# Optimization experiments

Hardware: AMD Instinct MI355X
Metric: run time of the kernel (lower is better)

## Reference

```python
import jax, jax.numpy as jnp
import numpy as np

I = 2048  # input_size
O = 2048  # output_size
K = 16    # number of parallel linears

def setup_inputs() -> dict:
    key = jax.random.key(0)
    ks = jax.random.split(key, 8)
    s_in = 1.0 / np.sqrt(I)
    s_cat = 1.0 / np.sqrt(K * O)
    x = jax.random.normal(ks[0], (4, 2048, I), dtype=jnp.float32)
    W16 = jax.random.uniform(ks[1], (K, O, I), jnp.float32, -s_in, s_in)   # stacked weights of 16 Linears
    b16 = jax.random.uniform(ks[2], (K, O), jnp.float32, -s_in, s_in)
    Wf = jax.random.uniform(ks[3], (O, K * O), jnp.float32, -s_cat, s_cat)  # fusion Linear weight
    bf = jax.random.uniform(ks[4], (O,), jnp.float32, -s_cat, s_cat)
    gamma = jnp.ones((O,), jnp.float32)  # LayerNorm weight
    beta = jnp.zeros((O,), jnp.float32)  # LayerNorm bias
    return {"x": x, "W16": W16, "b16": b16, "Wf": Wf, "bf": bf, "gamma": gamma, "beta": beta}

def reference(x, W16, b16, Wf, bf, gamma, beta):
    B, S, _ = x.shape
    # 16 parallel Linears as one batched GEMM; k index order == torch.cat order
    y = jnp.einsum('bsi,koi->bsko', x, W16) + b16          # [B,S,16,O]
    combined = y.reshape(B, S, K * O)                       # concat along last dim
    fused = jnp.einsum('bsc,oc->bso', combined, Wf) + bf    # fusion linear [B,S,O]
    # LayerNorm (eps=1e-5, torch default)
    mu = jnp.mean(fused, axis=-1, keepdims=True)
    var = jnp.mean(jnp.square(fused - mu), axis=-1, keepdims=True)
    normed = (fused - mu) * jax.lax.rsqrt(var + 1e-5) * gamma + beta
    # exact (erf) GELU matching torch nn.GELU default; dropout(p=0.005) is identity at eval
    return jax.nn.gelu(normed, approximate=False)
```

## Files before the change

kernel.cpp:

```cpp
#include <hip/hip_runtime.h>
#include <hip/hip_bf16.h>
#include <math.h>


typedef __bf16 bf16_t;
typedef __bf16 bf16x8 __attribute__((ext_vector_type(8)));
typedef __bf16 bf16x4 __attribute__((ext_vector_type(4)));
typedef float  f32x4  __attribute__((ext_vector_type(4)));

#define KC 32768
#define OD 2048
#define ID 2048
#define BSROWS 8192

#define GLL16(g, l) __builtin_amdgcn_global_load_lds( \
    (const __attribute__((address_space(1))) void*)(g), \
    (__attribute__((address_space(3))) void*)(l), 16, 0, 0)

__device__ __forceinline__ float wave_sum(float v) {
#pragma unroll
  for (int o = 32; o > 0; o >>= 1) v += __shfl_down(v, o, 64);
  return v;
}

__global__ __launch_bounds__(512, 1) void gemm256(
    const bf16_t* __restrict__ A, const bf16_t* __restrict__ B,
    float* __restrict__ C, int M, int N, int lda, int ldb,
    int Ks, int nbn, int mn)
{
  __shared__ char lds[131072];
  const int tid  = threadIdx.x;
  const int lane = tid & 63;
  const int wave = tid >> 6;

  const int nwg = gridDim.x;
  const int per = nwg >> 3;
  const int swz = (blockIdx.x & 7) * per + (blockIdx.x >> 3);
  const int z   = swz / mn;
  const int rem = swz - z * mn;
  const int bm  = (rem / nbn) * 256;
  const int bn  = (rem % nbn) * 256;
  const int k0  = z * Ks;
  float* Cz = C + (size_t)z * ((size_t)M * (size_t)N);

  const int wr = wave >> 2, wc = wave & 3;
  const int frow  = lane & 15;
  const int bhalf = wc >> 1;

  const int rdsl0 = (((lane >> 4))     ^ (lane & 7)) * 16;
  const int rdsl1 = (((lane >> 4) + 4) ^ (lane & 7)) * 16;

  const int abase = wr * 16384 + frow * 128;
  const int bloc  = ((wc & 1) * 64 + frow) * 128;

  const int srow8 = tid >> 3;
  const int sw8   = (tid & 7) ^ (srow8 & 7);
  const bf16_t* gA0 = A + (size_t)(bm + srow8) * lda + k0 + sw8 * 8;
  const bf16_t* gB0 = B + (size_t)(bn + srow8) * ldb + k0 + sw8 * 8;
  const int ldw = wave * 1024;

  f32x4 acc[8][4] = {};
  bf16x8 aqE[2][2], aqO[2][2], bA[4][2], bB[4][2];
  const int NT = Ks >> 6;

#define STAGE_A_HALF(t, hf) do {                                          \
    _Pragma("unroll") for (int s_ = 0; s_ < 2; ++s_)                      \
      GLL16(gA0 + (size_t)((hf) * 128 + s_ * 64) * lda + (size_t)(t) * 64,\
            lds + (((t) & 1) << 15) + (hf) * 16384 + s_ * 8192 + ldw);    \
  } while (0)

#define STAGE_B_HALF(t, hh) do {                                          \
    _Pragma("unroll") for (int s_ = 0; s_ < 2; ++s_)                      \
      GLL16(gB0 + (size_t)((hh) * 128 + s_ * 64) * ldb + (size_t)(t) * 64,\
            lds + 65536 + ((((t) * 2 + (hh)) & 3) << 14) + s_ * 8192 + ldw); \
  } while (0)

#define READ_AQ(t, q, aq) do {                                            \
    const char* p_ = lds + (((t) & 1) << 15) + abase + (q) * 4096;        \
    aq[0][0] = *reinterpret_cast<const bf16x8*>(p_ + rdsl0);              \
    aq[0][1] = *reinterpret_cast<const bf16x8*>(p_ + rdsl1);              \
    aq[1][0] = *reinterpret_cast<const bf16x8*>(p_ + 2048 + rdsl0);       \
    aq[1][1] = *reinterpret_cast<const bf16x8*>(p_ + 2048 + rdsl1);       \
  } while (0)

#define READ_BH(t, kh, bg) do {                                           \
    const char* p_ = lds + 65536 + ((((t) * 2 + bhalf) & 3) << 14) + bloc;\
    _Pragma("unroll") for (int n_ = 0; n_ < 4; ++n_)                      \
      bg[n_][kh] = *reinterpret_cast<const bf16x8*>(                      \
          p_ + n_ * 2048 + ((kh) ? rdsl1 : rdsl0));                       \
  } while (0)

#define SYNCPH() do {                                                     \
    __builtin_amdgcn_s_barrier();                                         \
    asm volatile("s_waitcnt lgkmcnt(0)" ::: "memory");                    \
    __builtin_amdgcn_sched_barrier(0);                                    \
  } while (0)

#define MFMA_Q(q, aq, bg) do {                                            \
    __builtin_amdgcn_s_setprio(1);                                        \
    _Pragma("unroll") for (int mh_ = 0; mh_ < 2; ++mh_)                   \
      _Pragma("unroll") for (int n_ = 0; n_ < 4; ++n_) {                  \
        acc[2*(q)+mh_][n_] = __builtin_amdgcn_mfma_f32_16x16x32_bf16(     \
            aq[mh_][0], bg[n_][0], acc[2*(q)+mh_][n_], 0, 0, 0);          \
        acc[2*(q)+mh_][n_] = __builtin_amdgcn_mfma_f32_16x16x32_bf16(     \
            aq[mh_][1], bg[n_][1], acc[2*(q)+mh_][n_], 0, 0, 0);          \
      }                                                                   \
    __builtin_amdgcn_s_setprio(0);                                        \
  } while (0)

#define TILE(t, BC, BN) do {                                              \
                                                                  \
    if ((t) + 1 < NT) { STAGE_A_HALF((t) + 1, 0); STAGE_A_HALF((t) + 1, 1); } \
    READ_AQ((t), 0, aqE);                                                 \
    SYNCPH(); MFMA_Q(0, aqE, BC);                                         \
                                                                  \
    READ_AQ((t), 1, aqO);                                                 \
    SYNCPH(); MFMA_Q(1, aqO, BC);                                         \
    if ((t) + 1 < NT) {                  \
      asm volatile("s_waitcnt vmcnt(4)" ::: "memory");                    \
      __builtin_amdgcn_s_barrier();                                       \
    }                                                                     \
                                                                  \
    if ((t) + 2 < NT) { STAGE_B_HALF((t) + 2, 0); STAGE_B_HALF((t) + 2, 1); } \
    READ_AQ((t), 2, aqE);                                                 \
    if ((t) + 1 < NT) READ_BH((t) + 1, 0, BN);                            \
    SYNCPH(); MFMA_Q(2, aqE, BC);                                         \
                                                                  \
    READ_AQ((t), 3, aqO);                                                 \
    if ((t) + 1 < NT) READ_BH((t) + 1, 1, BN);                            \
    SYNCPH(); MFMA_Q(3, aqO, BC);                                         \
    if ((t) + 2 < NT) {                  \
      asm volatile("s_waitcnt vmcnt(4)" ::: "memory");                    \
      __builtin_amdgcn_s_barrier();                                       \
    } else if ((t) + 1 < NT) {                                            \
      asm volatile("s_waitcnt vmcnt(0)" ::: "memory");    \
      __builtin_amdgcn_s_barrier();                                       \
    }                                                                     \
  } while (0)

  STAGE_A_HALF(0, 0); STAGE_A_HALF(0, 1);
  STAGE_B_HALF(0, 0); STAGE_B_HALF(0, 1);
  STAGE_B_HALF(1, 0); STAGE_B_HALF(1, 1);
  asm volatile("s_waitcnt vmcnt(4)" ::: "memory");
  __builtin_amdgcn_s_barrier();
  READ_BH(0, 0, bA);
  READ_BH(0, 1, bA);
  asm volatile("s_waitcnt lgkmcnt(0)" ::: "memory");
  __builtin_amdgcn_sched_barrier(0);
  __builtin_amdgcn_s_barrier();

#pragma unroll 1
  for (int t = 0; t < NT; t += 2) {
    TILE(t,     bA, bB);
    TILE(t + 1, bB, bA);
  }
#undef TILE
#undef MFMA_Q
#undef SYNCPH
#undef READ_BH
#undef READ_AQ
#undef STAGE_B_HALF
#undef STAGE_A_HALF

  const int wrbase = wr * 128, wcbase = wc * 64;
  const int cr = (lane >> 4) * 4, cc = lane & 15;
#pragma unroll
  for (int m = 0; m < 8; ++m)
#pragma unroll
    for (int n = 0; n < 4; ++n) {
      size_t base = (size_t)(bm + wrbase + m * 16 + cr) * N + (bn + wcbase + n * 16 + cc);
#pragma unroll
      for (int j = 0; j < 4; ++j)
        Cz[base + (size_t)j * N] = acc[m][n][j];
    }
}

#define PREP_WF_BLOCKS   32768
#define PREP_TR_BLOCKS   16384
#define PREP_X_BLOCKS    8192
#define PREP_TOTAL       (PREP_WF_BLOCKS + PREP_TR_BLOCKS + PREP_X_BLOCKS)

__global__ __launch_bounds__(256) void prep_all(
    const float* __restrict__ Wf, const float* __restrict__ b16,
    const float* __restrict__ W16, const float* __restrict__ X,
    bf16_t* __restrict__ Wf16, bf16_t* __restrict__ W16T,
    bf16_t* __restrict__ X16, float* __restrict__ beq)
{
  __shared__ bf16_t tile[64][65];
  const int b = blockIdx.x;
  const int t = threadIdx.x;

  if (b < PREP_WF_BLOCKS) {
    const int o  = b >> 4;
    const int cb = (b & 15) * 2048;
    const size_t gbase = (size_t)o * KC + cb + t * 8;
    const float4 v0 = *(const float4*)(Wf + gbase);
    const float4 v1 = *(const float4*)(Wf + gbase + 4);
    const float4 b0 = *(const float4*)(b16 + cb + t * 8);
    const float4 b1 = *(const float4*)(b16 + cb + t * 8 + 4);
    bf16x8 r;
    r[0] = (bf16_t)v0.x; r[1] = (bf16_t)v0.y; r[2] = (bf16_t)v0.z; r[3] = (bf16_t)v0.w;
    r[4] = (bf16_t)v1.x; r[5] = (bf16_t)v1.y; r[6] = (bf16_t)v1.z; r[7] = (bf16_t)v1.w;
    *reinterpret_cast<bf16x8*>(Wf16 + gbase) = r;
    float s = v0.x * b0.x + v0.y * b0.y + v0.z * b0.z + v0.w * b0.w
            + v1.x * b1.x + v1.y * b1.y + v1.z * b1.z + v1.w * b1.w;
    s = wave_sum(s);
    __shared__ float red[4];
    if ((t & 63) == 0) red[t >> 6] = s;
    __syncthreads();
    if (t == 0) atomicAdd(beq + o, red[0] + red[1] + red[2] + red[3]);
  } else if (b < PREP_WF_BLOCKS + PREP_TR_BLOCKS) {
    const int idx = b - PREP_WF_BLOCKS;
    const int cb = (idx & 511) * 64;
    const int ib = (idx >> 9) * 64;
    const int tx = t & 63;
    const int ty = t >> 6;
#pragma unroll
    for (int r = ty; r < 64; r += 4)
      tile[r][tx] = (bf16_t)W16[(size_t)(cb + r) * ID + ib + tx];
    __syncthreads();
    const int orow = t >> 3;
    const int oc8  = (t & 7) * 8;
#pragma unroll
    for (int rr = 0; rr < 2; ++rr) {
      const int r = orow + rr * 32;
      bf16x8 v;
#pragma unroll
      for (int j = 0; j < 8; ++j) v[j] = tile[oc8 + j][r];
      *reinterpret_cast<bf16x8*>(W16T + (size_t)(ib + r) * KC + cb + oc8) = v;
    }
  } else {
    const size_t i = ((size_t)(b - PREP_WF_BLOCKS - PREP_TR_BLOCKS) * 256 + t) * 8;
    const float4 v0 = *(const float4*)(X + i);
    const float4 v1 = *(const float4*)(X + i + 4);
    bf16x8 r;
    r[0] = (bf16_t)v0.x; r[1] = (bf16_t)v0.y; r[2] = (bf16_t)v0.z; r[3] = (bf16_t)v0.w;
    r[4] = (bf16_t)v1.x; r[5] = (bf16_t)v1.y; r[6] = (bf16_t)v1.z; r[7] = (bf16_t)v1.w;
    *reinterpret_cast<bf16x8*>(X16 + i) = r;
  }
}

__global__ void reduce_weq(const float* __restrict__ slabs, bf16_t* __restrict__ Weq)
{
  const size_t MN = (size_t)OD * ID;
  const size_t i = ((size_t)blockIdx.x * 256 + threadIdx.x) * 4;
  float4 a = *(const float4*)(slabs + i);
  float4 b = *(const float4*)(slabs + MN + i);
  float4 c = *(const float4*)(slabs + 2 * MN + i);
  float4 d = *(const float4*)(slabs + 3 * MN + i);
  bf16x4 r;
  r[0] = (bf16_t)(a.x + b.x + c.x + d.x);
  r[1] = (bf16_t)(a.y + b.y + c.y + d.y);
  r[2] = (bf16_t)(a.z + b.z + c.z + d.z);
  r[3] = (bf16_t)(a.w + b.w + c.w + d.w);
  *reinterpret_cast<bf16x4*>(Weq + i) = r;
}

__global__ __launch_bounds__(256) void ln_gelu(
    const float* __restrict__ fused, const float* __restrict__ beq,
    const float* __restrict__ bfv, const float* __restrict__ gamma,
    const float* __restrict__ beta, float* __restrict__ out)
{
  const int row = blockIdx.x;
  const int t = threadIdx.x;
  const float* fr = fused + (size_t)row * OD;
  const int c0 = t * 8;
  float v[8];
  float s = 0.f, ss = 0.f;
#pragma unroll
  for (int j = 0; j < 2; ++j) {
    float4 x  = *(const float4*)(fr  + c0 + j * 4);
    float4 bq = *(const float4*)(beq + c0 + j * 4);
    float4 bb = *(const float4*)(bfv + c0 + j * 4);
    v[j * 4 + 0] = x.x + bq.x + bb.x;
    v[j * 4 + 1] = x.y + bq.y + bb.y;
    v[j * 4 + 2] = x.z + bq.z + bb.z;
    v[j * 4 + 3] = x.w + bq.w + bb.w;
#pragma unroll
    for (int e = 0; e < 4; ++e) { float w = v[j * 4 + e]; s += w; ss += w * w; }
  }
  s = wave_sum(s); ss = wave_sum(ss);
  __shared__ float rs[4], rss[4];
  if ((t & 63) == 0) { rs[t >> 6] = s; rss[t >> 6] = ss; }
  __syncthreads();
  const float S  = rs[0] + rs[1] + rs[2] + rs[3];
  const float SS = rss[0] + rss[1] + rss[2] + rss[3];
  const float mu   = S * (1.f / OD);
  const float var  = SS * (1.f / OD) - mu * mu;
  const float rstd = rsqrtf(var + 1e-5f);
#pragma unroll
  for (int j = 0; j < 2; ++j) {
    float4 g  = *(const float4*)(gamma + c0 + j * 4);
    float4 be = *(const float4*)(beta  + c0 + j * 4);
    float4 o;
    float xn;
    xn  = (v[j * 4 + 0] - mu) * rstd * g.x + be.x; o.x = 0.5f * xn * (1.f + erff(xn * 0.70710678118f));
    xn  = (v[j * 4 + 1] - mu) * rstd * g.y + be.y; o.y = 0.5f * xn * (1.f + erff(xn * 0.70710678118f));
    xn  = (v[j * 4 + 2] - mu) * rstd * g.z + be.z; o.z = 0.5f * xn * (1.f + erff(xn * 0.70710678118f));
    xn  = (v[j * 4 + 3] - mu) * rstd * g.w + be.w; o.w = 0.5f * xn * (1.f + erff(xn * 0.70710678118f));
    *(float4*)(out + (size_t)row * OD + c0 + j * 4) = o;
  }
}

extern "C" void kernel_launch(void* const* d_in, const int* in_sizes, int n_in,
                              void* d_out, int out_size, void* d_ws, size_t ws_size,
                              hipStream_t stream) {
  const float* x     = (const float*)d_in[0];
  const float* W16   = (const float*)d_in[1];
  const float* b16   = (const float*)d_in[2];
  const float* Wf    = (const float*)d_in[3];
  const float* bfv   = (const float*)d_in[4];
  const float* gamma = (const float*)d_in[5];
  const float* beta  = (const float*)d_in[6];
  float* out = (float*)d_out;

  char* ws = (char*)d_ws;
  bf16_t* W16T  = (bf16_t*)(ws);
  bf16_t* Wf16  = (bf16_t*)(ws + 134217728);
  bf16_t* X16   = (bf16_t*)(ws + 268435456);
  bf16_t* Weq   = (bf16_t*)(ws + 301989888);
  float*  beq   = (float*)(ws + 310378496);
  float*  slabs = (float*)(ws + 310386688);
  float*  fused = slabs;

  hipMemsetAsync(beq, 0, OD * sizeof(float), stream);

  prep_all<<<PREP_TOTAL, 256, 0, stream>>>(Wf, b16, W16, x, Wf16, W16T, X16, beq);

  gemm256<<<256, 512, 0, stream>>>(Wf16, W16T, slabs, OD, ID, KC, KC, KC / 4, 8, 64);
  reduce_weq<<<(OD * ID) / (256 * 4), 256, 0, stream>>>(slabs, Weq);

  gemm256<<<256, 512, 0, stream>>>(X16, Weq, fused, BSROWS, OD, ID, ID, ID, 8, 256);

  ln_gelu<<<BSROWS, 256, 0, stream>>>(fused, beq, bfv, gamma, beta, out);
}
```

Before: 505.4 us.

## Restructure GEMM pipeline to triple-buffer A tiles and double-buffer B in LDS

```diff
diff --git a/kernel.cpp b/kernel.cpp
--- a/kernel.cpp
+++ b/kernel.cpp
@@ -28,7 +28,7 @@
     float* __restrict__ C, int M, int N, int lda, int ldb,
     int Ks, int nbn, int mn)
 {
-  __shared__ char lds[131072];
+  __shared__ char lds[163840];
   const int tid  = threadIdx.x;
   const int lane = tid & 63;
   const int wave = tid >> 6;
@@ -44,14 +44,13 @@
   float* Cz = C + (size_t)z * ((size_t)M * (size_t)N);
 
   const int wr = wave >> 2, wc = wave & 3;
-  const int frow  = lane & 15;
-  const int bhalf = wc >> 1;
+  const int frow = lane & 15;
 
   const int rdsl0 = (((lane >> 4))     ^ (lane & 7)) * 16;
   const int rdsl1 = (((lane >> 4) + 4) ^ (lane & 7)) * 16;
 
   const int abase = wr * 16384 + frow * 128;
-  const int bloc  = ((wc & 1) * 64 + frow) * 128;
+  const int bbase = (wc * 64 + frow) * 128;
 
   const int srow8 = tid >> 3;
   const int sw8   = (tid & 7) ^ (srow8 & 7);
@@ -60,34 +59,37 @@
   const int ldw = wave * 1024;
 
   f32x4 acc[8][4] = {};
-  bf16x8 aqE[2][2], aqO[2][2], bA[4][2], bB[4][2];
+  bf16x8 aqE[2][2], aqO[2][2], bg[4][2];
   const int NT = Ks >> 6;
 
-#define STAGE_A_HALF(t, hf) do {                                          \
-    _Pragma("unroll") for (int s_ = 0; s_ < 2; ++s_)                      \
-      GLL16(gA0 + (size_t)((hf) * 128 + s_ * 64) * lda + (size_t)(t) * 64,\
-            lds + (((t) & 1) << 15) + (hf) * 16384 + s_ * 8192 + ldw);    \
-  } while (0)
-
-#define STAGE_B_HALF(t, hh) do {                                          \
-    _Pragma("unroll") for (int s_ = 0; s_ < 2; ++s_)                      \
-      GLL16(gB0 + (size_t)((hh) * 128 + s_ * 64) * ldb + (size_t)(t) * 64,\
-            lds + 65536 + ((((t) * 2 + (hh)) & 3) << 14) + s_ * 8192 + ldw); \
-  } while (0)
-
-#define READ_AQ(t, q, aq) do {                                            \
-    const char* p_ = lds + (((t) & 1) << 15) + abase + (q) * 4096;        \
+#define STAGE_A(t, slot) do {                                             \
+    char* d_ = lds + (slot) * 32768;                                      \
+    const bf16_t* s_ = gA0 + (size_t)(t) * 64;                            \
+    _Pragma("unroll") for (int q_ = 0; q_ < 4; ++q_)                      \
+      GLL16(s_ + (size_t)(q_ * 64) * lda, d_ + q_ * 8192 + ldw);          \
+  } while (0)
+
+#define STAGE_B(t) do {                                                   \
+    char* d_ = lds + 98304 + (((t) & 1) << 15);                           \
+    const bf16_t* s_ = gB0 + (size_t)(t) * 64;                            \
+    _Pragma("unroll") for (int q_ = 0; q_ < 4; ++q_)                      \
+      GLL16(s_ + (size_t)(q_ * 64) * ldb, d_ + q_ * 8192 + ldw);          \
+  } while (0)
+
+#define READ_AQ(slot, q, aq) do {                                         \
+    const char* p_ = lds + (slot) * 32768 + abase + (q) * 4096;           \
     aq[0][0] = *reinterpret_cast<const bf16x8*>(p_ + rdsl0);              \
     aq[0][1] = *reinterpret_cast<const bf16x8*>(p_ + rdsl1);              \
     aq[1][0] = *reinterpret_cast<const bf16x8*>(p_ + 2048 + rdsl0);       \
     aq[1][1] = *reinterpret_cast<const bf16x8*>(p_ + 2048 + rdsl1);       \
   } while (0)
 
-#define READ_BH(t, kh, bg) do {                                           \
-    const char* p_ = lds + 65536 + ((((t) * 2 + bhalf) & 3) << 14) + bloc;\
-    _Pragma("unroll") for (int n_ = 0; n_ < 4; ++n_)                      \
-      bg[n_][kh] = *reinterpret_cast<const bf16x8*>(                      \
-          p_ + n_ * 2048 + ((kh) ? rdsl1 : rdsl0));                       \
+#define READ_B(t) do {                                                    \
+    const char* p_ = lds + 98304 + (((t) & 1) << 15) + bbase;             \
+    _Pragma("unroll") for (int n_ = 0; n_ < 4; ++n_) {                    \
+      bg[n_][0] = *reinterpret_cast<const bf16x8*>(p_ + n_ * 2048 + rdsl0); \
+      bg[n_][1] = *reinterpret_cast<const bf16x8*>(p_ + n_ * 2048 + rdsl1); \
+    }                                                                     \
   } while (0)
 
 #define SYNCPH() do {                                                     \
@@ -96,7 +98,7 @@
     __builtin_amdgcn_sched_barrier(0);                                    \
   } while (0)
 
-#define MFMA_Q(q, aq, bg) do {                                            \
+#define MFMA_Q(q, aq) do {                                                \
     __builtin_amdgcn_s_setprio(1);                                        \
     _Pragma("unroll") for (int mh_ = 0; mh_ < 2; ++mh_)                   \
       _Pragma("unroll") for (int n_ = 0; n_ < 4; ++n_) {                  \
@@ -108,59 +110,47 @@
     __builtin_amdgcn_s_setprio(0);                                        \
   } while (0)
 
-#define TILE(t, BC, BN) do {                                              \
-                                                                  \
-    if ((t) + 1 < NT) { STAGE_A_HALF((t) + 1, 0); STAGE_A_HALF((t) + 1, 1); } \
-    READ_AQ((t), 0, aqE);                                                 \
-    SYNCPH(); MFMA_Q(0, aqE, BC);                                         \
-                                                                  \
-    READ_AQ((t), 1, aqO);                                                 \
-    SYNCPH(); MFMA_Q(1, aqO, BC);                                         \
-    if ((t) + 1 < NT) {                  \
-      asm volatile("s_waitcnt vmcnt(4)" ::: "memory");                    \
-      __builtin_amdgcn_s_barrier();                                       \
-    }                                                                     \
-                                                                  \
-    if ((t) + 2 < NT) { STAGE_B_HALF((t) + 2, 0); STAGE_B_HALF((t) + 2, 1); } \
-    READ_AQ((t), 2, aqE);                                                 \
-    if ((t) + 1 < NT) READ_BH((t) + 1, 0, BN);                            \
-    SYNCPH(); MFMA_Q(2, aqE, BC);                                         \
-                                                                  \
-    READ_AQ((t), 3, aqO);                                                 \
-    if ((t) + 1 < NT) READ_BH((t) + 1, 1, BN);                            \
-    SYNCPH(); MFMA_Q(3, aqO, BC);                                         \
-    if ((t) + 2 < NT) {                  \
-      asm volatile("s_waitcnt vmcnt(4)" ::: "memory");                    \
-      __builtin_amdgcn_s_barrier();                                       \
-    } else if ((t) + 1 < NT) {                                            \
-      asm volatile("s_waitcnt vmcnt(0)" ::: "memory");    \
-      __builtin_amdgcn_s_barrier();                                       \
-    }                                                                     \
-  } while (0)
-
-  STAGE_A_HALF(0, 0); STAGE_A_HALF(0, 1);
-  STAGE_B_HALF(0, 0); STAGE_B_HALF(0, 1);
-  STAGE_B_HALF(1, 0); STAGE_B_HALF(1, 1);
+  STAGE_A(0, 0);
+  STAGE_B(0);
+  STAGE_A(1, 1);
   asm volatile("s_waitcnt vmcnt(4)" ::: "memory");
   __builtin_amdgcn_s_barrier();
-  READ_BH(0, 0, bA);
-  READ_BH(0, 1, bA);
-  asm volatile("s_waitcnt lgkmcnt(0)" ::: "memory");
-  __builtin_amdgcn_sched_barrier(0);
-  __builtin_amdgcn_s_barrier();
-
+
+  int sA = 0;
 #pragma unroll 1
-  for (int t = 0; t < NT; t += 2) {
-    TILE(t,     bA, bB);
-    TILE(t + 1, bB, bA);
+  for (int t = 0; t < NT; ++t) {
+    const int sA2 = (sA >= 1) ? sA - 1 : sA + 2;
+
+    if (t + 1 < NT) STAGE_B(t + 1);
+    READ_B(t);
+    READ_AQ(sA, 0, aqE);
+    SYNCPH(); MFMA_Q(0, aqE);
+
+    if (t + 2 < NT) STAGE_A(t + 2, sA2);
+    READ_AQ(sA, 1, aqO);
+    SYNCPH(); MFMA_Q(1, aqO);
+
+    READ_AQ(sA, 2, aqE);
+    SYNCPH(); MFMA_Q(2, aqE);
+
+    READ_AQ(sA, 3, aqO);
+    SYNCPH(); MFMA_Q(3, aqO);
+
+    if (t + 2 < NT) {
+      asm volatile("s_waitcnt vmcnt(4)" ::: "memory");
+      __builtin_amdgcn_s_barrier();
+    } else if (t + 1 < NT) {
+      asm volatile("s_waitcnt vmcnt(0)" ::: "memory");
+      __builtin_amdgcn_s_barrier();
+    }
+    sA = (sA >= 2) ? 0 : sA + 1;
   }
-#undef TILE
 #undef MFMA_Q
 #undef SYNCPH
-#undef READ_BH
+#undef READ_B
 #undef READ_AQ
-#undef STAGE_B_HALF
-#undef STAGE_A_HALF
+#undef STAGE_B
+#undef STAGE_A
 
   const int wrbase = wr * 128, wcbase = wc * 64;
   const int cr = (lane >> 4) * 4, cc = lane & 15;
```

New measurement: 506.7 us. About the same (+0.2%).
